# Performance work log

Hardware: AMD Instinct MI355X
Metric: run time of the kernel (lower is better)

Reference implementation:

```python
import jax, jax.numpy as jnp
import numpy as np

B, T, N_EMBD, HEAD = 8, 2048, 1024, 64

def setup_inputs() -> dict:
    key = jax.random.key(0)
    kx, kk, kq, kv = jax.random.split(key, 4)
    x = jax.random.normal(kx, (B, T, N_EMBD), dtype=jnp.float32)
    Wk = jax.random.normal(kk, (HEAD, N_EMBD), dtype=jnp.float32) * 0.02
    Wq = jax.random.normal(kq, (HEAD, N_EMBD), dtype=jnp.float32) * 0.02
    Wv = jax.random.normal(kv, (HEAD, N_EMBD), dtype=jnp.float32) * 0.02
    return {"x": x, "Wk": Wk, "Wq": Wq, "Wv": Wv}

def reference(x, Wk, Wq, Wv):
    # x: [B, T, C]; Linear(n_embd, head_size, bias=False) => x @ W.T
    Bq, Tq, C = x.shape
    q = jnp.einsum('btc,hc->bth', x, Wq)  # [B, T, H]
    k = jnp.einsum('btc,hc->bth', x, Wk)
    v = jnp.einsum('btc,hc->bth', x, Wv)
    # NOTE: source scales by C**0.5 with C = n_embd (not head_size); preserved.
    scale = 1.0 / jnp.sqrt(jnp.float32(C))
    wei = jnp.einsum('bth,bsh->bts', q, k) * scale  # [B, T, T]
    # causal mask: allow key position s <= query position t
    causal = jnp.tril(jnp.ones((Tq, Tq), dtype=bool))
    wei = jnp.where(causal[None, :, :], wei, -jnp.inf)
    wei = jax.nn.softmax(wei, axis=-1)
    # dropout is identity at inference
    out = jnp.einsum('bts,bsh->bth', wei, v)  # [B, T, H]
    return out
```

## Files before the change

### kernel.cpp

```cpp
#include <hip/hip_runtime.h>

#define TB 2048
#define NB 8
#define CEMB 1024
#define HD 64
#define BT (NB*TB)
#define QSCALE 0.04508422f

typedef __attribute__((ext_vector_type(8))) short bf16x8;
typedef __attribute__((ext_vector_type(4))) float f32x4;

__device__ inline short f2bf(float f) {
    union { float f; unsigned u; } v; v.f = f;
    unsigned r = v.u + 0x7fffu + ((v.u >> 16) & 1u);
    return (short)(r >> 16);
}
__device__ inline float bf2f(short s) {
    union { unsigned u; float f; } v; v.u = ((unsigned)(unsigned short)s) << 16;
    return v.f;
}

__global__ __launch_bounds__(256) void wpack(const float* __restrict__ Wk,
                                             const float* __restrict__ Wq,
                                             const float* __restrict__ Wv,
                                             short* __restrict__ W2) {
    int c = blockIdx.x * 256 + threadIdx.x;
    int lane = c & 63, ntk = c >> 6;
    int nt = ntk % 12, kc = ntk / 12;
    int n = nt * 16 + (lane & 15);
    int col = kc * 32 + (lane >> 4) * 8;
    const float* src = (n < 64) ? Wk + n * 1024
                     : (n < 128) ? Wq + (n - 64) * 1024
                                 : Wv + (n - 128) * 1024;
    float4 a = *(const float4*)(src + col);
    float4 b = *(const float4*)(src + col + 4);
    bf16x8 o;
    o[0] = f2bf(a.x); o[1] = f2bf(a.y); o[2] = f2bf(a.z); o[3] = f2bf(a.w);
    o[4] = f2bf(b.x); o[5] = f2bf(b.y); o[6] = f2bf(b.z); o[7] = f2bf(b.w);
    *(bf16x8*)(W2 + (size_t)c * 8) = o;
}

__global__ __launch_bounds__(256) void qkv_proj(const float* __restrict__ x,
                                                const short* __restrict__ W2,
                                                short* __restrict__ Qb,
                                                short* __restrict__ Kb,
                                                short* __restrict__ Vt) {
    __shared__ short4 Lred[4][3][3][64];
    int tid = threadIdx.x, wave = tid >> 6, lane = tid & 63;
    int l15 = lane & 15, quad = lane >> 4;
    int m0 = blockIdx.x * 16;
    int mrow = m0 + l15;

    f32x4 acc[12];
#pragma unroll
    for (int i = 0; i < 12; ++i) acc[i] = f32x4{0.f, 0.f, 0.f, 0.f};

    const float4* xb4 = (const float4*)(x + (size_t)mrow * CEMB + wave * 256) + quad * 2;
    float4 xr[16];
#pragma unroll
    for (int kc = 0; kc < 8; ++kc) {
        xr[2 * kc]     = xb4[kc * 8];
        xr[2 * kc + 1] = xb4[kc * 8 + 1];
    }
    __builtin_amdgcn_sched_barrier(0);

#pragma unroll
    for (int kc = 0; kc < 8; ++kc) {
        const short* wb = W2 + ((size_t)((wave * 8 + kc) * 12) * 64 + lane) * 8;
        bf16x8 wf[12];
#pragma unroll
        for (int nt = 0; nt < 12; ++nt)
            wf[nt] = *(const bf16x8*)(wb + nt * 512);
        float4 x0 = xr[2 * kc], x1 = xr[2 * kc + 1];
        bf16x8 af;
        af[0] = f2bf(x0.x); af[1] = f2bf(x0.y); af[2] = f2bf(x0.z); af[3] = f2bf(x0.w);
        af[4] = f2bf(x1.x); af[5] = f2bf(x1.y); af[6] = f2bf(x1.z); af[7] = f2bf(x1.w);
#pragma unroll
        for (int nt = 0; nt < 12; ++nt)
            acc[nt] = __builtin_amdgcn_mfma_f32_16x16x32_bf16(af, wf[nt], acc[nt], 0, 0, 0);
    }

#pragma unroll
    for (int nt = 0; nt < 12; ++nt) {
        int o = nt / 3;
        if (o != wave) {
            int rank = wave - (wave > o ? 1 : 0);
            short4 p;
            p.x = f2bf(acc[nt][0]); p.y = f2bf(acc[nt][1]);
            p.z = f2bf(acc[nt][2]); p.w = f2bf(acc[nt][3]);
            Lred[o][rank][nt % 3][lane] = p;
        }
    }
    __syncthreads();

    int b = blockIdx.x >> 7;
    int sblk = (m0 & 2047) >> 4;
#pragma unroll
    for (int nt = 0; nt < 12; ++nt) {
        if (wave == nt / 3) {
            f32x4 s = acc[nt];
#pragma unroll
            for (int rk = 0; rk < 3; ++rk) {
                short4 p = Lred[nt / 3][rk][nt % 3][lane];
                s[0] += bf2f(p.x); s[1] += bf2f(p.y);
                s[2] += bf2f(p.z); s[3] += bf2f(p.w);
            }
            if (nt < 4) {
                int h = nt * 16 + l15;
#pragma unroll
                for (int r = 0; r < 4; ++r)
                    Kb[(size_t)(m0 + quad * 4 + r) * HD + h] = f2bf(s[r]);
            } else if (nt < 8) {
                int h = (nt - 4) * 16 + l15;
#pragma unroll
                for (int r = 0; r < 4; ++r)
                    Qb[(size_t)(m0 + quad * 4 + r) * HD + h] = f2bf(s[r] * QSCALE);
            } else {
                int h = (nt - 8) * 16 + l15;
                short4 o4;
                o4.x = f2bf(s[0]); o4.y = f2bf(s[1]); o4.z = f2bf(s[2]); o4.w = f2bf(s[3]);
                *(short4*)(Vt + ((size_t)(b * 128 + sblk) * 64 + h) * 16 + quad * 4) = o4;
            }
        }
    }
}

#define PPAD 72
__global__ __launch_bounds__(256) void flash(const short* __restrict__ Qb,
                                             const short* __restrict__ Kb,
                                             const short* __restrict__ Vt,
                                             float* __restrict__ out) {
    __shared__ short U[4][2432];
    __shared__ float Ml[4][16];
    int tid = threadIdx.x, wave = tid >> 6, lane = tid & 63;
    int l15 = lane & 15, quad = lane >> 4;
    int i = blockIdx.x;
    int round = i >> 8, s = i & 255;
    int b = round * 2 + (s & 1);
    int q = (round & 1) ? 127 - (s >> 1) : (s >> 1);
    int tq0 = q * 16;
    size_t bT = (size_t)b * TB;

    const short* qrow = Qb + (bT + tq0 + l15) * HD;
    bf16x8 qf0 = *(const bf16x8*)(qrow + quad * 8);
    bf16x8 qf1 = *(const bf16x8*)(qrow + 32 + quad * 8);

    bf16x8 onesf;
#pragma unroll
    for (int j = 0; j < 8; ++j) onesf[j] = (short)0x3F80;

    f32x4 accO[4];
#pragma unroll
    for (int k = 0; k < 4; ++k) accO[k] = f32x4{0.f, 0.f, 0.f, 0.f};
    f32x4 accL = f32x4{0.f, 0.f, 0.f, 0.f};

    int ntiles = (q + 4) >> 2;
    const short* kbase = Kb + bT * HD;
    const short* vtb = Vt + (size_t)b * 131072;
    short* Psh = U[wave];

    int myt = wave;
    if (myt < ntiles) {
        bf16x8 kf[8];
        {
            const short* kr = kbase + (size_t)(myt * 64 + l15) * HD + quad * 8;
#pragma unroll
            for (int st = 0; st < 4; ++st) {
                kf[st * 2]     = *(const bf16x8*)(kr + (size_t)st * 16 * HD);
                kf[st * 2 + 1] = *(const bf16x8*)(kr + (size_t)st * 16 * HD + 32);
            }
        }
        for (; myt < ntiles; myt += 4) {
            int s0 = myt * 64;
            bf16x8 vf[8];
            {
                int sb = (s0 >> 4) + (quad >> 1);
                int so = (quad & 1) * 8;
#pragma unroll
                for (int ht = 0; ht < 4; ++ht) {
                    vf[ht * 2]     = *(const bf16x8*)(vtb + (sb * 64 + ht * 16 + l15) * 16 + so);
                    vf[ht * 2 + 1] = *(const bf16x8*)(vtb + ((sb + 2) * 64 + ht * 16 + l15) * 16 + so);
                }
            }
            f32x4 sv[4];
#pragma unroll
            for (int st = 0; st < 4; ++st) {
                f32x4 sacc = f32x4{0.f, 0.f, 0.f, 0.f};
                sacc = __builtin_amdgcn_mfma_f32_16x16x32_bf16(qf0, kf[st * 2], sacc, 0, 0, 0);
                sacc = __builtin_amdgcn_mfma_f32_16x16x32_bf16(qf1, kf[st * 2 + 1], sacc, 0, 0, 0);
                sv[st] = sacc;
            }
            if (myt + 4 < ntiles) {
                const short* kr = kbase + (size_t)(s0 + 256 + l15) * HD + quad * 8;
#pragma unroll
                for (int st = 0; st < 4; ++st) {
                    kf[st * 2]     = *(const bf16x8*)(kr + (size_t)st * 16 * HD);
                    kf[st * 2 + 1] = *(const bf16x8*)(kr + (size_t)st * 16 * HD + 32);
                }
            }
            bool full = (s0 + 64 <= tq0);
#pragma unroll
            for (int r = 0; r < 4; ++r) {
                int tg = tq0 + quad * 4 + r;
                float e0, e1, e2, e3;
                if (full) {
                    e0 = __builtin_amdgcn_exp2f(sv[0][r]);
                    e1 = __builtin_amdgcn_exp2f(sv[1][r]);
                    e2 = __builtin_amdgcn_exp2f(sv[2][r]);
                    e3 = __builtin_amdgcn_exp2f(sv[3][r]);
                } else {
                    int sg = s0 + l15;
                    e0 = (sg      <= tg) ? __builtin_amdgcn_exp2f(sv[0][r]) : 0.f;
                    e1 = (sg + 16 <= tg) ? __builtin_amdgcn_exp2f(sv[1][r]) : 0.f;
                    e2 = (sg + 32 <= tg) ? __builtin_amdgcn_exp2f(sv[2][r]) : 0.f;
                    e3 = (sg + 48 <= tg) ? __builtin_amdgcn_exp2f(sv[3][r]) : 0.f;
                }
                int prow = (quad * 4 + r) * PPAD;
                Psh[prow + l15]      = f2bf(e0);
                Psh[prow + 16 + l15] = f2bf(e1);
                Psh[prow + 32 + l15] = f2bf(e2);
                Psh[prow + 48 + l15] = f2bf(e3);
            }
            asm volatile("s_waitcnt lgkmcnt(0)" ::: "memory");
            bf16x8 pf0 = *(const bf16x8*)&Psh[l15 * PPAD + quad * 8];
            bf16x8 pf1 = *(const bf16x8*)&Psh[l15 * PPAD + 32 + quad * 8];
            accL = __builtin_amdgcn_mfma_f32_16x16x32_bf16(pf0, onesf, accL, 0, 0, 0);
            accL = __builtin_amdgcn_mfma_f32_16x16x32_bf16(pf1, onesf, accL, 0, 0, 0);
#pragma unroll
            for (int ht = 0; ht < 4; ++ht) {
                accO[ht] = __builtin_amdgcn_mfma_f32_16x16x32_bf16(pf0, vf[ht * 2], accO[ht], 0, 0, 0);
                accO[ht] = __builtin_amdgcn_mfma_f32_16x16x32_bf16(pf1, vf[ht * 2 + 1], accO[ht], 0, 0, 0);
            }
        }
    }

    float* of = (float*)U[wave];
#pragma unroll
    for (int ht = 0; ht < 4; ++ht)
#pragma unroll
        for (int r = 0; r < 4; ++r)
            of[(quad * 4 + r) * 68 + ht * 16 + l15] = accO[ht][r];
    if (l15 == 0) {
#pragma unroll
        for (int r = 0; r < 4; ++r)
            Ml[wave][quad * 4 + r] = accL[r];
    }
    __syncthreads();

    int row = tid >> 4, c4 = (tid & 15) * 4;
    float L = Ml[0][row] + Ml[1][row] + Ml[2][row] + Ml[3][row];
    float inv = 1.0f / L;
    float4 p0 = *(const float4*)((const float*)U[0] + row * 68 + c4);
    float4 p1 = *(const float4*)((const float*)U[1] + row * 68 + c4);
    float4 p2 = *(const float4*)((const float*)U[2] + row * 68 + c4);
    float4 p3 = *(const float4*)((const float*)U[3] + row * 68 + c4);
    float4 o;
    o.x = (p0.x + p1.x + p2.x + p3.x) * inv;
    o.y = (p0.y + p1.y + p2.y + p3.y) * inv;
    o.z = (p0.z + p1.z + p2.z + p3.z) * inv;
    o.w = (p0.w + p1.w + p2.w + p3.w) * inv;
    *(float4*)(out + (bT + tq0 + row) * HD + c4) = o;
}

extern "C" void kernel_launch(void* const* d_in, const int* in_sizes, int n_in,
                              void* d_out, int out_size, void* d_ws, size_t ws_size,
                              hipStream_t stream) {
    const float* x  = (const float*)d_in[0];
    const float* Wk = (const float*)d_in[1];
    const float* Wq = (const float*)d_in[2];
    const float* Wv = (const float*)d_in[3];
    float* out = (float*)d_out;

    short* W2 = (short*)d_ws;
    short* Qb = W2 + 192 * 1024;
    short* Kb = Qb + (size_t)BT * HD;
    short* Vt = Kb + (size_t)BT * HD;

    wpack<<<96, 256, 0, stream>>>(Wk, Wq, Wv, W2);
    qkv_proj<<<1024, 256, 0, stream>>>(x, W2, Qb, Kb, Vt);
    flash<<<1024, 256, 0, stream>>>(Qb, Kb, Vt, out);
}
```

Before: 146.3 us.

## Keep P in registers via transposed S MFMA and software-pipeline QKV projection loads

The flash kernel now computes S transposed (K as the A operand), so the exponentiated P values already sit in the B-operand layout of 16x16x16 MFMAs. The P round-trip through LDS and its waitcnt are dropped, and P·V and the row sums are accumulated directly from registers. The projection kernel double-buffers the weight fragments and rotates three x slices, so loads for the next k-chunk overlap the current MFMAs. The cost is twice as many smaller MFMA instructions, narrower V loads, and higher register pressure.

Measured after the change: 156.6 us. 1.07x slower.

```diff
diff --git a/kernel.cpp b/kernel.cpp
--- a/kernel.cpp
+++ b/kernel.cpp
@@ -8,7 +8,11 @@
 #define QSCALE 0.04508422f
 
 typedef __attribute__((ext_vector_type(8))) short bf16x8;
+typedef __attribute__((ext_vector_type(4))) short bf16x4;
 typedef __attribute__((ext_vector_type(4))) float f32x4;
+
+#define MFMA32(a, b, c) __builtin_amdgcn_mfma_f32_16x16x32_bf16(a, b, c, 0, 0, 0)
+#define MFMA16(a, b, c) __builtin_amdgcn_mfma_f32_16x16x16bf16_1k(a, b, c, 0, 0, 0)
 
 __device__ inline short f2bf(float f) {
     union { float f; unsigned u; } v; v.f = f;
@@ -56,28 +60,44 @@
     for (int i = 0; i < 12; ++i) acc[i] = f32x4{0.f, 0.f, 0.f, 0.f};
 
     const float4* xb4 = (const float4*)(x + (size_t)mrow * CEMB + wave * 256) + quad * 2;
-    float4 xr[16];
+    float4 xq[6];
+    xq[0] = xb4[0];  xq[1] = xb4[1];
+    xq[2] = xb4[8];  xq[3] = xb4[9];
+    xq[4] = xb4[16]; xq[5] = xb4[17];
+
+    const short* wbase = W2 + ((size_t)(wave * 8) * 12 * 64 + lane) * 8;
+    bf16x8 wA[12], wB[12];
+#pragma unroll
+    for (int nt = 0; nt < 12; ++nt)
+        wA[nt] = *(const bf16x8*)(wbase + nt * 512);
+
 #pragma unroll
     for (int kc = 0; kc < 8; ++kc) {
-        xr[2 * kc]     = xb4[kc * 8];
-        xr[2 * kc + 1] = xb4[kc * 8 + 1];
-    }
-    __builtin_amdgcn_sched_barrier(0);
-
-#pragma unroll
-    for (int kc = 0; kc < 8; ++kc) {
-        const short* wb = W2 + ((size_t)((wave * 8 + kc) * 12) * 64 + lane) * 8;
-        bf16x8 wf[12];
-#pragma unroll
-        for (int nt = 0; nt < 12; ++nt)
-            wf[nt] = *(const bf16x8*)(wb + nt * 512);
-        float4 x0 = xr[2 * kc], x1 = xr[2 * kc + 1];
+        float4 x0 = xq[(kc % 3) * 2], x1 = xq[(kc % 3) * 2 + 1];
+        if (kc + 1 < 8) {
+            const short* wn = wbase + (size_t)(kc + 1) * 6144;
+            if (kc & 1) {
+#pragma unroll
+                for (int nt = 0; nt < 12; ++nt) wA[nt] = *(const bf16x8*)(wn + nt * 512);
+            } else {
+#pragma unroll
+                for (int nt = 0; nt < 12; ++nt) wB[nt] = *(const bf16x8*)(wn + nt * 512);
+            }
+        }
+        if (kc + 3 < 8) {
+            xq[((kc + 3) % 3) * 2]     = xb4[(kc + 3) * 8];
+            xq[((kc + 3) % 3) * 2 + 1] = xb4[(kc + 3) * 8 + 1];
+        }
         bf16x8 af;
         af[0] = f2bf(x0.x); af[1] = f2bf(x0.y); af[2] = f2bf(x0.z); af[3] = f2bf(x0.w);
         af[4] = f2bf(x1.x); af[5] = f2bf(x1.y); af[6] = f2bf(x1.z); af[7] = f2bf(x1.w);
-#pragma unroll
-        for (int nt = 0; nt < 12; ++nt)
-            acc[nt] = __builtin_amdgcn_mfma_f32_16x16x32_bf16(af, wf[nt], acc[nt], 0, 0, 0);
+        if (kc & 1) {
+#pragma unroll
+            for (int nt = 0; nt < 12; ++nt) acc[nt] = MFMA32(af, wB[nt], acc[nt]);
+        } else {
+#pragma unroll
+            for (int nt = 0; nt < 12; ++nt) acc[nt] = MFMA32(af, wA[nt], acc[nt]);
+        }
     }
 
 #pragma unroll
@@ -125,12 +145,11 @@
     }
 }
 
-#define PPAD 72
 __global__ __launch_bounds__(256) void flash(const short* __restrict__ Qb,
                                              const short* __restrict__ Kb,
                                              const short* __restrict__ Vt,
                                              float* __restrict__ out) {
-    __shared__ short U[4][2432];
+    __shared__ float Of[4][16][68];
     __shared__ float Ml[4][16];
     int tid = threadIdx.x, wave = tid >> 6, lane = tid & 63;
     int l15 = lane & 15, quad = lane >> 4;
@@ -145,9 +164,9 @@
     bf16x8 qf0 = *(const bf16x8*)(qrow + quad * 8);
     bf16x8 qf1 = *(const bf16x8*)(qrow + 32 + quad * 8);
 
-    bf16x8 onesf;
-#pragma unroll
-    for (int j = 0; j < 8; ++j) onesf[j] = (short)0x3F80;
+    bf16x4 ones4;
+#pragma unroll
+    for (int j = 0; j < 4; ++j) ones4[j] = (short)0x3F80;
 
     f32x4 accO[4];
 #pragma unroll
@@ -157,7 +176,6 @@
     int ntiles = (q + 4) >> 2;
     const short* kbase = Kb + bT * HD;
     const short* vtb = Vt + (size_t)b * 131072;
-    short* Psh = U[wave];
 
     int myt = wave;
     if (myt < ntiles) {
@@ -172,22 +190,20 @@
         }
         for (; myt < ntiles; myt += 4) {
             int s0 = myt * 64;
-            bf16x8 vf[8];
-            {
-                int sb = (s0 >> 4) + (quad >> 1);
-                int so = (quad & 1) * 8;
-#pragma unroll
-                for (int ht = 0; ht < 4; ++ht) {
-                    vf[ht * 2]     = *(const bf16x8*)(vtb + (sb * 64 + ht * 16 + l15) * 16 + so);
-                    vf[ht * 2 + 1] = *(const bf16x8*)(vtb + ((sb + 2) * 64 + ht * 16 + l15) * 16 + so);
-                }
+            bf16x4 vf[16];
+#pragma unroll
+            for (int g = 0; g < 4; ++g) {
+                int sb = (s0 >> 4) + g;
+#pragma unroll
+                for (int ht = 0; ht < 4; ++ht)
+                    vf[g * 4 + ht] = *(const bf16x4*)(vtb + ((size_t)(sb * 64 + ht * 16 + l15)) * 16 + quad * 4);
             }
             f32x4 sv[4];
 #pragma unroll
             for (int st = 0; st < 4; ++st) {
                 f32x4 sacc = f32x4{0.f, 0.f, 0.f, 0.f};
-                sacc = __builtin_amdgcn_mfma_f32_16x16x32_bf16(qf0, kf[st * 2], sacc, 0, 0, 0);
-                sacc = __builtin_amdgcn_mfma_f32_16x16x32_bf16(qf1, kf[st * 2 + 1], sacc, 0, 0, 0);
+                sacc = MFMA32(kf[st * 2], qf0, sacc);
+                sacc = MFMA32(kf[st * 2 + 1], qf1, sacc);
                 sv[st] = sacc;
             }
             if (myt + 4 < ntiles) {
@@ -199,61 +215,43 @@
                 }
             }
             bool full = (s0 + 64 <= tq0);
-#pragma unroll
-            for (int r = 0; r < 4; ++r) {
-                int tg = tq0 + quad * 4 + r;
-                float e0, e1, e2, e3;
-                if (full) {
-                    e0 = __builtin_amdgcn_exp2f(sv[0][r]);
-                    e1 = __builtin_amdgcn_exp2f(sv[1][r]);
-                    e2 = __builtin_amdgcn_exp2f(sv[2][r]);
-                    e3 = __builtin_amdgcn_exp2f(sv[3][r]);
-                } else {
-                    int sg = s0 + l15;
-                    e0 = (sg      <= tg) ? __builtin_amdgcn_exp2f(sv[0][r]) : 0.f;
-                    e1 = (sg + 16 <= tg) ? __builtin_amdgcn_exp2f(sv[1][r]) : 0.f;
-                    e2 = (sg + 32 <= tg) ? __builtin_amdgcn_exp2f(sv[2][r]) : 0.f;
-                    e3 = (sg + 48 <= tg) ? __builtin_amdgcn_exp2f(sv[3][r]) : 0.f;
+            int tg = tq0 + l15;
+            bf16x4 pk[4];
+#pragma unroll
+            for (int st = 0; st < 4; ++st) {
+#pragma unroll
+                for (int r = 0; r < 4; ++r) {
+                    int sg = s0 + st * 16 + quad * 4 + r;
+                    float e = (full || sg <= tg) ? __builtin_amdgcn_exp2f(sv[st][r]) : 0.f;
+                    pk[st][r] = f2bf(e);
                 }
-                int prow = (quad * 4 + r) * PPAD;
-                Psh[prow + l15]      = f2bf(e0);
-                Psh[prow + 16 + l15] = f2bf(e1);
-                Psh[prow + 32 + l15] = f2bf(e2);
-                Psh[prow + 48 + l15] = f2bf(e3);
-            }
-            asm volatile("s_waitcnt lgkmcnt(0)" ::: "memory");
-            bf16x8 pf0 = *(const bf16x8*)&Psh[l15 * PPAD + quad * 8];
-            bf16x8 pf1 = *(const bf16x8*)&Psh[l15 * PPAD + 32 + quad * 8];
-            accL = __builtin_amdgcn_mfma_f32_16x16x32_bf16(pf0, onesf, accL, 0, 0, 0);
-            accL = __builtin_amdgcn_mfma_f32_16x16x32_bf16(pf1, onesf, accL, 0, 0, 0);
-#pragma unroll
-            for (int ht = 0; ht < 4; ++ht) {
-                accO[ht] = __builtin_amdgcn_mfma_f32_16x16x32_bf16(pf0, vf[ht * 2], accO[ht], 0, 0, 0);
-                accO[ht] = __builtin_amdgcn_mfma_f32_16x16x32_bf16(pf1, vf[ht * 2 + 1], accO[ht], 0, 0, 0);
-            }
-        }
-    }
-
-    float* of = (float*)U[wave];
-#pragma unroll
-    for (int ht = 0; ht < 4; ++ht)
-#pragma unroll
-        for (int r = 0; r < 4; ++r)
-            of[(quad * 4 + r) * 68 + ht * 16 + l15] = accO[ht][r];
-    if (l15 == 0) {
-#pragma unroll
-        for (int r = 0; r < 4; ++r)
-            Ml[wave][quad * 4 + r] = accL[r];
-    }
+            }
+#pragma unroll
+            for (int g = 0; g < 4; ++g) {
+                accL = MFMA16(ones4, pk[g], accL);
+#pragma unroll
+                for (int ht = 0; ht < 4; ++ht)
+                    accO[ht] = MFMA16(vf[g * 4 + ht], pk[g], accO[ht]);
+            }
+        }
+    }
+
+#pragma unroll
+    for (int ht = 0; ht < 4; ++ht) {
+        float4 o4;
+        o4.x = accO[ht][0]; o4.y = accO[ht][1]; o4.z = accO[ht][2]; o4.w = accO[ht][3];
+        *(float4*)&Of[wave][l15][ht * 16 + quad * 4] = o4;
+    }
+    if (quad == 0) Ml[wave][l15] = accL[0];
     __syncthreads();
 
     int row = tid >> 4, c4 = (tid & 15) * 4;
     float L = Ml[0][row] + Ml[1][row] + Ml[2][row] + Ml[3][row];
     float inv = 1.0f / L;
-    float4 p0 = *(const float4*)((const float*)U[0] + row * 68 + c4);
-    float4 p1 = *(const float4*)((const float*)U[1] + row * 68 + c4);
-    float4 p2 = *(const float4*)((const float*)U[2] + row * 68 + c4);
-    float4 p3 = *(const float4*)((const float*)U[3] + row * 68 + c4);
+    float4 p0 = *(const float4*)&Of[0][row][c4];
+    float4 p1 = *(const float4*)&Of[1][row][c4];
+    float4 p2 = *(const float4*)&Of[2][row][c4];
+    float4 p3 = *(const float4*)&Of[3][row][c4];
     float4 o;
     o.x = (p0.x + p1.x + p2.x + p3.x) * inv;
     o.y = (p0.y + p1.y + p2.y + p3.y) * inv;
```
